# Kernel optimization log

Measured on AMD Instinct MI355X. Metric: run time of the kernel, lower is better.

## Reference

```python
import jax, jax.numpy as jnp
import numpy as np

NUM_HEADS = 8
HEAD_DIM = 64  # joiner_dim 512 / 8
LN_EPS = 1e-5


def _layer_norm(x, g, b):
    mu = jnp.mean(x, axis=-1, keepdims=True)
    var = jnp.mean(jnp.square(x - mu), axis=-1, keepdims=True)
    return (x - mu) * jax.lax.rsqrt(var + LN_EPS) * g + b


def setup_inputs() -> dict:
    key = jax.random.key(0)
    ks = jax.random.split(key, 24)
    N, T, S = 16, 512, 5
    E, D, J, V = 512, 512, 512, 2000
    s = 0.02
    inp = {
        "encoder_out": jax.random.normal(ks[0], (N, T, S, E), jnp.float32),
        "decoder_out": jax.random.normal(ks[1], (N, T, S, D), jnp.float32),
        # ScaledLinear projections (initial_scale absorbed into weights)
        "We": jax.random.normal(ks[2], (J, E), jnp.float32) * s * 0.25,
        "be": jnp.zeros((J,), jnp.float32),
        "Wd": jax.random.normal(ks[3], (J, D), jnp.float32) * s * 0.25,
        "bd": jnp.zeros((J,), jnp.float32),
        # LayerNorms
        "g_q": jnp.ones((J,), jnp.float32),
        "beta_q": jnp.zeros((J,), jnp.float32),
        "g_kv": jnp.ones((J,), jnp.float32),
        "beta_kv": jnp.zeros((J,), jnp.float32),
        # attention projections (xavier-ish)
        "Wq": jax.random.normal(ks[4], (J, J), jnp.float32) * s,
        "bq": jnp.zeros((J,), jnp.float32),
        "Wk": jax.random.normal(ks[5], (J, J), jnp.float32) * s,
        "bk": jnp.zeros((J,), jnp.float32),
        "Wv": jax.random.normal(ks[6], (J, J), jnp.float32) * s,
        "bv": jnp.zeros((J,), jnp.float32),
        "Wo": jax.random.normal(ks[7], (J, J), jnp.float32) * s,
        "bo": jnp.zeros((J,), jnp.float32),
        # final vocab projection
        "Wout": jax.random.normal(ks[8], (V, J), jnp.float32) * s,
        "bout": jnp.zeros((V,), jnp.float32),
    }
    return inp


def reference(encoder_out, decoder_out, We, be, Wd, bd, g_q, beta_q, g_kv, beta_kv,
              Wq, bq, Wk, bk, Wv, bv, Wo, bo, Wout, bout):
    # input projections (mode == "transducer", project_input=True)
    enc = jnp.einsum('ntsc,jc->ntsj', encoder_out, We) + be
    dec = jnp.einsum('ntsc,jc->ntsj', decoder_out, Wd) + bd

    # framewise sigmoid attention
    q_in = _layer_norm(dec, g_q, beta_q)
    kv_in = _layer_norm(enc, g_kv, beta_kv)
    q = jnp.einsum('ntsj,kj->ntsk', q_in, Wq) + bq
    k = jnp.einsum('ntsj,kj->ntsk', kv_in, Wk) + bk
    v = jnp.einsum('ntsj,kj->ntsk', kv_in, Wv) + bv

    shp = q.shape[:-1]
    q = q.reshape(*shp, NUM_HEADS, HEAD_DIM)
    k = k.reshape(*shp, NUM_HEADS, HEAD_DIM)
    v = v.reshape(*shp, NUM_HEADS, HEAD_DIM)

    scale = HEAD_DIM ** -0.5
    attn = jax.nn.sigmoid(jnp.sum(q * k, axis=-1, keepdims=True) * scale)  # (N,T,S,H,1)
    context = (attn * v).reshape(*shp, NUM_HEADS * HEAD_DIM)
    context = jnp.einsum('ntsj,kj->ntsk', context, Wo) + bo

    h = jnp.tanh(dec + context)
    logits = jnp.einsum('ntsj,vj->ntsv', h, Wout) + bout
    return logits
```

## Files before the change

kernel.cpp:

```cpp
#include <hip/hip_runtime.h>
#include <stdint.h>


typedef __attribute__((ext_vector_type(8))) __bf16 bf16x8;
typedef __attribute__((ext_vector_type(4))) float float4v;
typedef __attribute__((ext_vector_type(8))) unsigned short ushort8;

static constexpr int M_TOT = 16 * 512 * 5;
static constexpr int JDIM  = 512;
static constexpr int VOUT  = 2000;
static constexpr int VPAD  = 2048;

#define DI __device__ __forceinline__

DI float bf2f(unsigned short u) {
    union { unsigned int i; float f; } w; w.i = ((unsigned int)u) << 16; return w.f;
}
DI unsigned short f2bf(float f) {
    union { float f; unsigned int i; } w; w.f = f;
    return (unsigned short)((w.i + 0x8000u) >> 16);
}

DI void gld_lds16(const void* g, void* l) {
    __builtin_amdgcn_global_load_lds(
        reinterpret_cast<__attribute__((address_space(1))) void*>(
            reinterpret_cast<uintptr_t>(g)),
        reinterpret_cast<__attribute__((address_space(3))) void*>(
            reinterpret_cast<uintptr_t>(l)),
        16, 0, 0);
}

template <int EPI, int NOUT, bool A32>
__global__ __launch_bounds__(256) void gemm_bt(
    const void* __restrict__ Ap, const unsigned short* __restrict__ B,
    const float* __restrict__ bias, void* __restrict__ Cp,
    const unsigned short* __restrict__ dres,
    float* __restrict__ st_sum, float* __restrict__ st_ssq,
    const float* __restrict__ rs)
{
    constexpr int K = 512;
    constexpr int BM = 128, BN = 128, BK = 32;
    __shared__ unsigned short As[BM * BK];
    __shared__ unsigned short Bs[BN * BK];

    const int tid  = threadIdx.x;
    const int wave = tid >> 6;
    const int lane = tid & 63;
    const int wm   = wave >> 1;
    const int wn   = wave & 1;
    const int quad = lane >> 4;
    const int l16  = lane & 15;

    const int gx      = gridDim.x;
    const int nwg     = gx * gridDim.y;
    const int id      = blockIdx.x + gx * blockIdx.y;
    const int logical = (id & 7) * (nwg >> 3) + (id >> 3);
    const int m0 = (logical / gx) * BM;
    const int n0 = (logical % gx) * BN;

    float4v acc[4][4];
#pragma unroll
    for (int i = 0; i < 4; i++)
#pragma unroll
        for (int j = 0; j < 4; j++)
            acc[i][j] = {0.f, 0.f, 0.f, 0.f};

    const float*          Af = (const float*)Ap;
    const unsigned short* Ab = (const unsigned short*)Ap;

    const int c0 = tid, c1 = tid + 256;
    const int ar0 = c0 >> 2, ac0 = (c0 & 3) * 8;
    const int ar1 = c1 >> 2, ac1 = (c1 & 3) * 8;

    for (int k0 = 0; k0 < K; k0 += BK) {
        gld_lds16(&B[(size_t)(n0 + ar0) * K + k0 + ac0], &Bs[c0 * 8]);
        gld_lds16(&B[(size_t)(n0 + ar1) * K + k0 + ac1], &Bs[c1 * 8]);
        if constexpr (A32) {
            const float* p0 = &Af[(size_t)(m0 + ar0) * K + k0 + ac0];
            const float* p1 = &Af[(size_t)(m0 + ar1) * K + k0 + ac1];
            float4 f0 = *(const float4*)p0;
            float4 f1 = *(const float4*)(p0 + 4);
            float4 g0 = *(const float4*)p1;
            float4 g1 = *(const float4*)(p1 + 4);
            ushort8 u0, u1;
            u0[0] = f2bf(f0.x); u0[1] = f2bf(f0.y); u0[2] = f2bf(f0.z); u0[3] = f2bf(f0.w);
            u0[4] = f2bf(f1.x); u0[5] = f2bf(f1.y); u0[6] = f2bf(f1.z); u0[7] = f2bf(f1.w);
            u1[0] = f2bf(g0.x); u1[1] = f2bf(g0.y); u1[2] = f2bf(g0.z); u1[3] = f2bf(g0.w);
            u1[4] = f2bf(g1.x); u1[5] = f2bf(g1.y); u1[6] = f2bf(g1.z); u1[7] = f2bf(g1.w);
            *reinterpret_cast<ushort8*>(&As[c0 * 8]) = u0;
            *reinterpret_cast<ushort8*>(&As[c1 * 8]) = u1;
        } else {
            gld_lds16(&Ab[(size_t)(m0 + ar0) * K + k0 + ac0], &As[c0 * 8]);
            gld_lds16(&Ab[(size_t)(m0 + ar1) * K + k0 + ac1], &As[c1 * 8]);
        }
        __syncthreads();

        bf16x8 af[4], bfv[4];
#pragma unroll
        for (int i = 0; i < 4; i++)
            af[i] = *reinterpret_cast<const bf16x8*>(
                &As[(wm * 64 + i * 16 + l16) * BK + quad * 8]);
#pragma unroll
        for (int j = 0; j < 4; j++)
            bfv[j] = *reinterpret_cast<const bf16x8*>(
                &Bs[(wn * 64 + j * 16 + l16) * BK + quad * 8]);
#pragma unroll
        for (int i = 0; i < 4; i++)
#pragma unroll
            for (int j = 0; j < 4; j++)
                acc[i][j] = __builtin_amdgcn_mfma_f32_16x16x32_bf16(
                    af[i], bfv[j], acc[i][j], 0, 0, 0);
        __syncthreads();
    }

    float bias_v[4], rs_v[4];
#pragma unroll
    for (int j = 0; j < 4; j++) {
        int col = n0 + wn * 64 + j * 16 + l16;
        bias_v[j] = (col < NOUT) ? bias[col] : 0.f;
        if constexpr (EPI == 4) rs_v[j] = rs[col];
    }

    if constexpr (EPI == 4) {
#pragma unroll
        for (int i = 0; i < 4; i++) {
            int rbase = m0 + wm * 64 + i * 16 + quad * 4;
#pragma unroll
            for (int r = 0; r < 4; r++) {
                int row = rbase + r;
                float s  = st_sum[row];
                float s2 = st_ssq[row];
                float mean = s * (1.f / 512.f);
                float var  = s2 * (1.f / 512.f) - mean * mean;
                float rstd = rsqrtf(var + 1e-5f);
                float crow = -mean * rstd;
#pragma unroll
                for (int j = 0; j < 4; j++) {
                    int col = n0 + wn * 64 + j * 16 + l16;
                    float val = fmaf(rstd, acc[i][j][r],
                                fmaf(crow, rs_v[j], bias_v[j]));
                    ((unsigned short*)Cp)[(size_t)row * NOUT + col] = f2bf(val);
                }
            }
        }
    } else {
#pragma unroll
        for (int i = 0; i < 4; i++) {
            int rbase = m0 + wm * 64 + i * 16 + quad * 4;
#pragma unroll
            for (int j = 0; j < 4; j++) {
                int col = n0 + wn * 64 + j * 16 + l16;
#pragma unroll
                for (int r = 0; r < 4; r++) {
                    float val = acc[i][j][r] + bias_v[j];
                    int row = rbase + r;
                    if constexpr (EPI == 2) {
                        float d = bf2f(dres[(size_t)row * 512 + col]);
                        ((unsigned short*)Cp)[(size_t)row * 512 + col] = f2bf(tanhf(d + val));
                    } else if constexpr (EPI == 3) {
                        if (col < NOUT)
                            ((float*)Cp)[(size_t)row * NOUT + col] = val;
                    } else {
                        ((unsigned short*)Cp)[(size_t)row * NOUT + col] = f2bf(val);
                    }
                }
            }
        }
    }

    if constexpr (EPI == 6) {
#pragma unroll
        for (int i = 0; i < 4; i++) {
#pragma unroll
            for (int r = 0; r < 4; r++) {
                float ps = 0.f, ps2 = 0.f;
#pragma unroll
                for (int j = 0; j < 4; j++) {
                    float v = acc[i][j][r] + bias_v[j];
                    ps += v;
                    ps2 = fmaf(v, v, ps2);
                }
#pragma unroll
                for (int m = 1; m < 16; m <<= 1) {
                    ps  += __shfl_xor(ps,  m, 64);
                    ps2 += __shfl_xor(ps2, m, 64);
                }
                if (l16 == 0) {
                    int row = m0 + wm * 64 + i * 16 + quad * 4 + r;
                    atomicAdd(&st_sum[row], ps);
                    atomicAdd(&st_ssq[row], ps2);
                }
            }
        }
    }
}

__global__ __launch_bounds__(256) void wconv_kernel(
    const float* __restrict__ We, const float* __restrict__ Wd,
    const float* __restrict__ Wq, const float* __restrict__ Wk,
    const float* __restrict__ Wv, const float* __restrict__ Wo,
    const float* __restrict__ Wout,
    const float* __restrict__ g_q, const float* __restrict__ g_kv,
    unsigned short* __restrict__ WB, float* __restrict__ stz)
{
#pragma unroll
    for (int t = 0; t < 4; t++) {
        int i = blockIdx.x * 1024 + t * 256 + threadIdx.x;
        float v;
        if (i < 1572864) {
            int seg = i >> 18, off = i & 262143;
            const float* src = seg == 0 ? We : seg == 1 ? Wd : seg == 2 ? Wq
                             : seg == 3 ? Wk : seg == 4 ? Wv : Wo;
            v = src[off];
            int j = off & 511;
            if (seg == 2)                 v *= g_q[j];
            else if (seg == 3 || seg == 4) v *= g_kv[j];
        } else {
            int rem = i - 1572864;
            int row = rem >> 9;
            v = (row < VOUT) ? Wout[rem] : 0.f;
        }
        WB[i] = f2bf(v);
    }
    int z = blockIdx.x * 256 + threadIdx.x;
    if (z < 163840) stz[z] = 0.f;
}

__global__ __launch_bounds__(256) void lnprep_kernel(
    const float* __restrict__ Wq, const float* __restrict__ Wk,
    const float* __restrict__ Wv,
    const float* __restrict__ g_q, const float* __restrict__ beta_q,
    const float* __restrict__ g_kv, const float* __restrict__ beta_kv,
    const float* __restrict__ bq, const float* __restrict__ bk,
    const float* __restrict__ bv,
    float* __restrict__ rs_q, float* __restrict__ b_q,
    float* __restrict__ rs_kv, float* __restrict__ b_kv)
{
    int idx  = blockIdx.x * 4 + (threadIdx.x >> 6);
    int lane = threadIdx.x & 63;
    const float *W, *g, *bt, *bb; float *rs_out, *b_out; int r;
    if (idx < 512)       { W = Wq; g = g_q;  bt = beta_q;  bb = bq;
                           rs_out = &rs_q[idx];        b_out = &b_q[idx];        r = idx; }
    else if (idx < 1024) { W = Wk; g = g_kv; bt = beta_kv; bb = bk;
                           rs_out = &rs_kv[idx - 512]; b_out = &b_kv[idx - 512]; r = idx - 512; }
    else                 { W = Wv; g = g_kv; bt = beta_kv; bb = bv;
                           rs_out = &rs_kv[idx - 512]; b_out = &b_kv[idx - 512]; r = idx - 1024; }

    const float* wr = &W[(size_t)r * 512];
    float s = 0.f, sb = 0.f;
    int j0 = lane * 8;
    float4 w0 = *(const float4*)&wr[j0];
    float4 w1 = *(const float4*)&wr[j0 + 4];
    float4 ga = *(const float4*)&g[j0];
    float4 gb = *(const float4*)&g[j0 + 4];
    float4 ba = *(const float4*)&bt[j0];
    float4 bb4 = *(const float4*)&bt[j0 + 4];
    s  += w0.x * ga.x + w0.y * ga.y + w0.z * ga.z + w0.w * ga.w;
    s  += w1.x * gb.x + w1.y * gb.y + w1.z * gb.z + w1.w * gb.w;
    sb += w0.x * ba.x + w0.y * ba.y + w0.z * ba.z + w0.w * ba.w;
    sb += w1.x * bb4.x + w1.y * bb4.y + w1.z * bb4.z + w1.w * bb4.w;
#pragma unroll
    for (int m = 1; m < 64; m <<= 1) {
        s  += __shfl_xor(s,  m, 64);
        sb += __shfl_xor(sb, m, 64);
    }
    if (lane == 0) { *rs_out = s; *b_out = bb[r] + sb; }
}

__global__ __launch_bounds__(256) void attn_kernel(
    const unsigned short* __restrict__ q, const unsigned short* __restrict__ kv,
    unsigned short* __restrict__ ctx)
{
    int row  = blockIdx.x * 4 + (threadIdx.x >> 6);
    int lane = threadIdx.x & 63;
    size_t qoff = (size_t)row * 512 + lane * 8;
    size_t kvo  = (size_t)row * 1024 + lane * 8;
    ushort8 uq = *reinterpret_cast<const ushort8*>(&q[qoff]);
    ushort8 uk = *reinterpret_cast<const ushort8*>(&kv[kvo]);
    float dot = 0.f;
#pragma unroll
    for (int j = 0; j < 8; j++) dot += bf2f(uq[j]) * bf2f(uk[j]);
    dot += __shfl_xor(dot, 1, 64);
    dot += __shfl_xor(dot, 2, 64);
    dot += __shfl_xor(dot, 4, 64);
    float sg = 1.f / (1.f + __expf(-dot * 0.125f));
    ushort8 uv = *reinterpret_cast<const ushort8*>(&kv[kvo + 512]);
    ushort8 o;
#pragma unroll
    for (int j = 0; j < 8; j++) o[j] = f2bf(sg * bf2f(uv[j]));
    *reinterpret_cast<ushort8*>(&ctx[qoff]) = o;
}

extern "C" void kernel_launch(void* const* d_in, const int* in_sizes, int n_in,
                              void* d_out, int out_size, void* d_ws, size_t ws_size,
                              hipStream_t stream)
{
    (void)in_sizes; (void)n_in; (void)out_size; (void)ws_size;
    const float* enc_in  = (const float*)d_in[0];
    const float* dec_in  = (const float*)d_in[1];
    const float* We      = (const float*)d_in[2];  const float* be     = (const float*)d_in[3];
    const float* Wd      = (const float*)d_in[4];  const float* bd     = (const float*)d_in[5];
    const float* g_q     = (const float*)d_in[6];  const float* beta_q = (const float*)d_in[7];
    const float* g_kv    = (const float*)d_in[8];  const float* beta_kv= (const float*)d_in[9];
    const float* Wq      = (const float*)d_in[10]; const float* bq     = (const float*)d_in[11];
    const float* Wk      = (const float*)d_in[12]; const float* bk     = (const float*)d_in[13];
    const float* Wv      = (const float*)d_in[14]; const float* bv     = (const float*)d_in[15];
    const float* Wo      = (const float*)d_in[16]; const float* bo     = (const float*)d_in[17];
    const float* Wout    = (const float*)d_in[18]; const float* bout   = (const float*)d_in[19];
    float* out = (float*)d_out;

    unsigned short* WB    = (unsigned short*)d_ws;
    unsigned short* WeB   = WB + 0;
    unsigned short* WdB   = WB + 262144;
    unsigned short* WqB   = WB + 524288;
    unsigned short* WkB   = WB + 786432;
    unsigned short* WoB   = WB + 1310720;
    unsigned short* WoutB = WB + 1572864;

    char* sbase = (char*)d_ws + 5242880;
    const size_t SZ = (size_t)M_TOT * 512 * 2;
    unsigned short* S0 = (unsigned short*)(sbase + 0 * SZ);
    unsigned short* S1 = (unsigned short*)(sbase + 1 * SZ);
    unsigned short* S2 = (unsigned short*)(sbase + 2 * SZ);
    unsigned short* S3 = (unsigned short*)(sbase + 3 * SZ);
    unsigned short* S4 = (unsigned short*)(sbase + 4 * SZ);
    unsigned short* S5 = (unsigned short*)(sbase + 5 * SZ);

    float* stf  = (float*)(sbase + 5 * SZ);
    float* sumD = stf;
    float* ssqD = stf + 40960;
    float* sumE = stf + 81920;
    float* ssqE = stf + 122880;
    float* rs_q  = stf + 163840;
    float* b_q   = stf + 164352;
    float* rs_kv = stf + 164864;
    float* b_kv  = stf + 165888;

    dim3 blk(256);
    dim3 g512(JDIM / 128, M_TOT / 128);
    dim3 g1024(1024 / 128, M_TOT / 128);
    dim3 gout(VPAD / 128, M_TOT / 128);

    wconv_kernel<<<2560, blk, 0, stream>>>(We, Wd, Wq, Wk, Wv, Wo, Wout,
                                           g_q, g_kv, WB, stf);
    lnprep_kernel<<<384, blk, 0, stream>>>(Wq, Wk, Wv, g_q, beta_q, g_kv, beta_kv,
                                           bq, bk, bv, rs_q, b_q, rs_kv, b_kv);

    gemm_bt<6, 512, true><<<g512, blk, 0, stream>>>(enc_in, WeB, be, S0, nullptr,
                                                    sumE, ssqE, nullptr);
    gemm_bt<6, 512, true><<<g512, blk, 0, stream>>>(dec_in, WdB, bd, S1, nullptr,
                                                    sumD, ssqD, nullptr);

    gemm_bt<4, 512, false><<<g512, blk, 0, stream>>>(S1, WqB, b_q, S4, nullptr,
                                                     sumD, ssqD, rs_q);
    gemm_bt<4, 1024, false><<<g1024, blk, 0, stream>>>(S0, WkB, b_kv, S2, nullptr,
                                                       sumE, ssqE, rs_kv);

    attn_kernel<<<M_TOT / 4, blk, 0, stream>>>(S4, S2, S5);

    gemm_bt<2, 512, false><<<g512, blk, 0, stream>>>(S5, WoB, bo, S3, S1,
                                                     nullptr, nullptr, nullptr);

    gemm_bt<3, 2000, false><<<gout, blk, 0, stream>>>(S3, WoutB, bout, out, nullptr,
                                                      nullptr, nullptr, nullptr);
}
```

Before: 888.5 us.

## Pre-convert encoder/decoder inputs to bf16 in a merged prep kernel

Merges the weight-conversion and LN-prep kernels into one prep kernel that also converts the fp32 encoder and decoder inputs to bf16 buffers. The input-projection GEMMs can then stage A through direct global-to-LDS loads instead of fp32 register loads with inline conversion. The block swizzle becomes a template option and is kept only for the vocab GEMM. The cost is an extra full write and read of bf16 copies of both inputs, plus two more workspace buffers.

```diff
diff --git a/kernel.cpp b/kernel.cpp
--- a/kernel.cpp
+++ b/kernel.cpp
@@ -30,9 +30,9 @@
         16, 0, 0);
 }
 
-template <int EPI, int NOUT, bool A32>
+template <int EPI, int NOUT, bool SWZ>
 __global__ __launch_bounds__(256) void gemm_bt(
-    const void* __restrict__ Ap, const unsigned short* __restrict__ B,
+    const unsigned short* __restrict__ A, const unsigned short* __restrict__ B,
     const float* __restrict__ bias, void* __restrict__ Cp,
     const unsigned short* __restrict__ dres,
     float* __restrict__ st_sum, float* __restrict__ st_ssq,
@@ -51,10 +51,15 @@
     const int quad = lane >> 4;
     const int l16  = lane & 15;
 
-    const int gx      = gridDim.x;
-    const int nwg     = gx * gridDim.y;
-    const int id      = blockIdx.x + gx * blockIdx.y;
-    const int logical = (id & 7) * (nwg >> 3) + (id >> 3);
+    const int gx = gridDim.x;
+    const int id = blockIdx.x + gx * blockIdx.y;
+    int logical;
+    if constexpr (SWZ) {
+        const int nwg = gx * gridDim.y;
+        logical = (id & 7) * (nwg >> 3) + (id >> 3);
+    } else {
+        logical = id;
+    }
     const int m0 = (logical / gx) * BM;
     const int n0 = (logical % gx) * BN;
 
@@ -64,9 +69,6 @@
 #pragma unroll
         for (int j = 0; j < 4; j++)
             acc[i][j] = {0.f, 0.f, 0.f, 0.f};
-
-    const float*          Af = (const float*)Ap;
-    const unsigned short* Ab = (const unsigned short*)Ap;
 
     const int c0 = tid, c1 = tid + 256;
     const int ar0 = c0 >> 2, ac0 = (c0 & 3) * 8;
@@ -75,24 +77,8 @@
     for (int k0 = 0; k0 < K; k0 += BK) {
         gld_lds16(&B[(size_t)(n0 + ar0) * K + k0 + ac0], &Bs[c0 * 8]);
         gld_lds16(&B[(size_t)(n0 + ar1) * K + k0 + ac1], &Bs[c1 * 8]);
-        if constexpr (A32) {
-            const float* p0 = &Af[(size_t)(m0 + ar0) * K + k0 + ac0];
-            const float* p1 = &Af[(size_t)(m0 + ar1) * K + k0 + ac1];
-            float4 f0 = *(const float4*)p0;
-            float4 f1 = *(const float4*)(p0 + 4);
-            float4 g0 = *(const float4*)p1;
-            float4 g1 = *(const float4*)(p1 + 4);
-            ushort8 u0, u1;
-            u0[0] = f2bf(f0.x); u0[1] = f2bf(f0.y); u0[2] = f2bf(f0.z); u0[3] = f2bf(f0.w);
-            u0[4] = f2bf(f1.x); u0[5] = f2bf(f1.y); u0[6] = f2bf(f1.z); u0[7] = f2bf(f1.w);
-            u1[0] = f2bf(g0.x); u1[1] = f2bf(g0.y); u1[2] = f2bf(g0.z); u1[3] = f2bf(g0.w);
-            u1[4] = f2bf(g1.x); u1[5] = f2bf(g1.y); u1[6] = f2bf(g1.z); u1[7] = f2bf(g1.w);
-            *reinterpret_cast<ushort8*>(&As[c0 * 8]) = u0;
-            *reinterpret_cast<ushort8*>(&As[c1 * 8]) = u1;
-        } else {
-            gld_lds16(&Ab[(size_t)(m0 + ar0) * K + k0 + ac0], &As[c0 * 8]);
-            gld_lds16(&Ab[(size_t)(m0 + ar1) * K + k0 + ac1], &As[c1 * 8]);
-        }
+        gld_lds16(&A[(size_t)(m0 + ar0) * K + k0 + ac0], &As[c0 * 8]);
+        gld_lds16(&A[(size_t)(m0 + ar1) * K + k0 + ac1], &As[c1 * 8]);
         __syncthreads();
 
         bf16x8 af[4], bfv[4];
@@ -195,76 +181,105 @@
     }
 }
 
-__global__ __launch_bounds__(256) void wconv_kernel(
+__global__ __launch_bounds__(256) void prep_kernel(
     const float* __restrict__ We, const float* __restrict__ Wd,
     const float* __restrict__ Wq, const float* __restrict__ Wk,
     const float* __restrict__ Wv, const float* __restrict__ Wo,
     const float* __restrict__ Wout,
-    const float* __restrict__ g_q, const float* __restrict__ g_kv,
-    unsigned short* __restrict__ WB, float* __restrict__ stz)
-{
-#pragma unroll
-    for (int t = 0; t < 4; t++) {
-        int i = blockIdx.x * 1024 + t * 256 + threadIdx.x;
-        float v;
-        if (i < 1572864) {
-            int seg = i >> 18, off = i & 262143;
-            const float* src = seg == 0 ? We : seg == 1 ? Wd : seg == 2 ? Wq
-                             : seg == 3 ? Wk : seg == 4 ? Wv : Wo;
-            v = src[off];
-            int j = off & 511;
-            if (seg == 2)                 v *= g_q[j];
-            else if (seg == 3 || seg == 4) v *= g_kv[j];
-        } else {
-            int rem = i - 1572864;
-            int row = rem >> 9;
-            v = (row < VOUT) ? Wout[rem] : 0.f;
-        }
-        WB[i] = f2bf(v);
-    }
-    int z = blockIdx.x * 256 + threadIdx.x;
-    if (z < 163840) stz[z] = 0.f;
-}
-
-__global__ __launch_bounds__(256) void lnprep_kernel(
-    const float* __restrict__ Wq, const float* __restrict__ Wk,
-    const float* __restrict__ Wv,
     const float* __restrict__ g_q, const float* __restrict__ beta_q,
     const float* __restrict__ g_kv, const float* __restrict__ beta_kv,
     const float* __restrict__ bq, const float* __restrict__ bk,
     const float* __restrict__ bv,
+    const float* __restrict__ enc_in, const float* __restrict__ dec_in,
+    unsigned short* __restrict__ WB,
+    unsigned short* __restrict__ encB, unsigned short* __restrict__ decB,
+    float* __restrict__ stz,
     float* __restrict__ rs_q, float* __restrict__ b_q,
     float* __restrict__ rs_kv, float* __restrict__ b_kv)
 {
-    int idx  = blockIdx.x * 4 + (threadIdx.x >> 6);
-    int lane = threadIdx.x & 63;
-    const float *W, *g, *bt, *bb; float *rs_out, *b_out; int r;
-    if (idx < 512)       { W = Wq; g = g_q;  bt = beta_q;  bb = bq;
-                           rs_out = &rs_q[idx];        b_out = &b_q[idx];        r = idx; }
-    else if (idx < 1024) { W = Wk; g = g_kv; bt = beta_kv; bb = bk;
-                           rs_out = &rs_kv[idx - 512]; b_out = &b_kv[idx - 512]; r = idx - 512; }
-    else                 { W = Wv; g = g_kv; bt = beta_kv; bb = bv;
-                           rs_out = &rs_kv[idx - 512]; b_out = &b_kv[idx - 512]; r = idx - 1024; }
-
-    const float* wr = &W[(size_t)r * 512];
-    float s = 0.f, sb = 0.f;
-    int j0 = lane * 8;
-    float4 w0 = *(const float4*)&wr[j0];
-    float4 w1 = *(const float4*)&wr[j0 + 4];
-    float4 ga = *(const float4*)&g[j0];
-    float4 gb = *(const float4*)&g[j0 + 4];
-    float4 ba = *(const float4*)&bt[j0];
-    float4 bb4 = *(const float4*)&bt[j0 + 4];
-    s  += w0.x * ga.x + w0.y * ga.y + w0.z * ga.z + w0.w * ga.w;
-    s  += w1.x * gb.x + w1.y * gb.y + w1.z * gb.z + w1.w * gb.w;
-    sb += w0.x * ba.x + w0.y * ba.y + w0.z * ba.z + w0.w * ba.w;
-    sb += w1.x * bb4.x + w1.y * bb4.y + w1.z * bb4.z + w1.w * bb4.w;
-#pragma unroll
-    for (int m = 1; m < 64; m <<= 1) {
-        s  += __shfl_xor(s,  m, 64);
-        sb += __shfl_xor(sb, m, 64);
-    }
-    if (lane == 0) { *rs_out = s; *b_out = bb[r] + sb; }
+    const int b   = blockIdx.x;
+    const int tid = threadIdx.x;
+
+    if (b < 1280) {
+        if (b < 768) {
+            const int seg = b >> 7;
+            const int off = (b & 127) * 2048 + tid * 8;
+            const float* src = seg == 0 ? We : seg == 1 ? Wd : seg == 2 ? Wq
+                             : seg == 3 ? Wk : seg == 4 ? Wv : Wo;
+            float4 f0 = *(const float4*)&src[off];
+            float4 f1 = *(const float4*)&src[off + 4];
+            float sc[8] = {1,1,1,1,1,1,1,1};
+            if (seg >= 2 && seg <= 4) {
+                const float* g = (seg == 2) ? g_q : g_kv;
+                int j0 = off & 511;
+                float4 s0 = *(const float4*)&g[j0];
+                float4 s1 = *(const float4*)&g[j0 + 4];
+                sc[0]=s0.x; sc[1]=s0.y; sc[2]=s0.z; sc[3]=s0.w;
+                sc[4]=s1.x; sc[5]=s1.y; sc[6]=s1.z; sc[7]=s1.w;
+            }
+            ushort8 u;
+            u[0]=f2bf(f0.x*sc[0]); u[1]=f2bf(f0.y*sc[1]); u[2]=f2bf(f0.z*sc[2]); u[3]=f2bf(f0.w*sc[3]);
+            u[4]=f2bf(f1.x*sc[4]); u[5]=f2bf(f1.y*sc[5]); u[6]=f2bf(f1.z*sc[6]); u[7]=f2bf(f1.w*sc[7]);
+            *reinterpret_cast<ushort8*>(&WB[(size_t)b * 2048 + tid * 8]) = u;
+        } else {
+            const int rem = (b - 768) * 2048 + tid * 8;
+            const int row = rem >> 9;
+            ushort8 u;
+            if (row < VOUT) {
+                float4 f0 = *(const float4*)&Wout[rem];
+                float4 f1 = *(const float4*)&Wout[rem + 4];
+                u[0]=f2bf(f0.x); u[1]=f2bf(f0.y); u[2]=f2bf(f0.z); u[3]=f2bf(f0.w);
+                u[4]=f2bf(f1.x); u[5]=f2bf(f1.y); u[6]=f2bf(f1.z); u[7]=f2bf(f1.w);
+            } else {
+                u = (ushort8)0;
+            }
+            *reinterpret_cast<ushort8*>(&WB[1572864 + (size_t)(b - 768) * 2048 + tid * 8]) = u;
+        }
+        int z = b * 256 + tid;
+        if (z < 163840) stz[z] = 0.f;
+    } else if (b < 21760) {
+        const bool isDec = b >= 11520;
+        const int  cb    = b - (isDec ? 11520 : 1280);
+        const float* src = isDec ? dec_in : enc_in;
+        unsigned short* dst = isDec ? decB : encB;
+        const size_t base = (size_t)cb * 2048 + tid * 8;
+        float4 f0 = *(const float4*)&src[base];
+        float4 f1 = *(const float4*)&src[base + 4];
+        ushort8 u;
+        u[0]=f2bf(f0.x); u[1]=f2bf(f0.y); u[2]=f2bf(f0.z); u[3]=f2bf(f0.w);
+        u[4]=f2bf(f1.x); u[5]=f2bf(f1.y); u[6]=f2bf(f1.z); u[7]=f2bf(f1.w);
+        *reinterpret_cast<ushort8*>(&dst[base]) = u;
+    } else {
+        const int idx  = (b - 21760) * 4 + (tid >> 6);
+        const int lane = tid & 63;
+        const float *W, *g, *bt, *bb; float *rs_out, *b_out; int r;
+        if (idx < 512)       { W = Wq; g = g_q;  bt = beta_q;  bb = bq;
+                               rs_out = &rs_q[idx];        b_out = &b_q[idx];        r = idx; }
+        else if (idx < 1024) { W = Wk; g = g_kv; bt = beta_kv; bb = bk;
+                               rs_out = &rs_kv[idx - 512]; b_out = &b_kv[idx - 512]; r = idx - 512; }
+        else                 { W = Wv; g = g_kv; bt = beta_kv; bb = bv;
+                               rs_out = &rs_kv[idx - 512]; b_out = &b_kv[idx - 512]; r = idx - 1024; }
+
+        const float* wr = &W[(size_t)r * 512];
+        float s = 0.f, sb = 0.f;
+        int j0 = lane * 8;
+        float4 w0 = *(const float4*)&wr[j0];
+        float4 w1 = *(const float4*)&wr[j0 + 4];
+        float4 ga = *(const float4*)&g[j0];
+        float4 gb = *(const float4*)&g[j0 + 4];
+        float4 ba = *(const float4*)&bt[j0];
+        float4 bb4 = *(const float4*)&bt[j0 + 4];
+        s  += w0.x * ga.x + w0.y * ga.y + w0.z * ga.z + w0.w * ga.w;
+        s  += w1.x * gb.x + w1.y * gb.y + w1.z * gb.z + w1.w * gb.w;
+        sb += w0.x * ba.x + w0.y * ba.y + w0.z * ba.z + w0.w * ba.w;
+        sb += w1.x * bb4.x + w1.y * bb4.y + w1.z * bb4.z + w1.w * bb4.w;
+#pragma unroll
+        for (int m = 1; m < 64; m <<= 1) {
+            s  += __shfl_xor(s,  m, 64);
+            sb += __shfl_xor(sb, m, 64);
+        }
+        if (lane == 0) { *rs_out = s; *b_out = bb[r] + sb; }
+    }
 }
 
 __global__ __launch_bounds__(256) void attn_kernel(
@@ -319,18 +334,20 @@
 
     char* sbase = (char*)d_ws + 5242880;
     const size_t SZ = (size_t)M_TOT * 512 * 2;
-    unsigned short* S0 = (unsigned short*)(sbase + 0 * SZ);
-    unsigned short* S1 = (unsigned short*)(sbase + 1 * SZ);
-    unsigned short* S2 = (unsigned short*)(sbase + 2 * SZ);
-    unsigned short* S3 = (unsigned short*)(sbase + 3 * SZ);
-    unsigned short* S4 = (unsigned short*)(sbase + 4 * SZ);
-    unsigned short* S5 = (unsigned short*)(sbase + 5 * SZ);
-
-    float* stf  = (float*)(sbase + 5 * SZ);
-    float* sumD = stf;
-    float* ssqD = stf + 40960;
-    float* sumE = stf + 81920;
-    float* ssqE = stf + 122880;
+    unsigned short* EB = (unsigned short*)(sbase + 0 * SZ);
+    unsigned short* DB = (unsigned short*)(sbase + 1 * SZ);
+    unsigned short* S0 = (unsigned short*)(sbase + 2 * SZ);
+    unsigned short* S1 = (unsigned short*)(sbase + 3 * SZ);
+    unsigned short* S2 = (unsigned short*)(sbase + 4 * SZ);
+    unsigned short* S3 = (unsigned short*)(sbase + 5 * SZ);
+    unsigned short* S4 = (unsigned short*)(sbase + 6 * SZ);
+    unsigned short* S5 = (unsigned short*)(sbase + 7 * SZ);
+
+    float* stf  = (float*)(sbase + 7 * SZ);
+    float* sumE = stf;
+    float* ssqE = stf + 40960;
+    float* sumD = stf + 81920;
+    float* ssqD = stf + 122880;
     float* rs_q  = stf + 163840;
     float* b_q   = stf + 164352;
     float* rs_kv = stf + 164864;
@@ -341,15 +358,14 @@
     dim3 g1024(1024 / 128, M_TOT / 128);
     dim3 gout(VPAD / 128, M_TOT / 128);
 
-    wconv_kernel<<<2560, blk, 0, stream>>>(We, Wd, Wq, Wk, Wv, Wo, Wout,
-                                           g_q, g_kv, WB, stf);
-    lnprep_kernel<<<384, blk, 0, stream>>>(Wq, Wk, Wv, g_q, beta_q, g_kv, beta_kv,
-                                           bq, bk, bv, rs_q, b_q, rs_kv, b_kv);
-
-    gemm_bt<6, 512, true><<<g512, blk, 0, stream>>>(enc_in, WeB, be, S0, nullptr,
-                                                    sumE, ssqE, nullptr);
-    gemm_bt<6, 512, true><<<g512, blk, 0, stream>>>(dec_in, WdB, bd, S1, nullptr,
-                                                    sumD, ssqD, nullptr);
+    prep_kernel<<<22144, blk, 0, stream>>>(
+        We, Wd, Wq, Wk, Wv, Wo, Wout, g_q, beta_q, g_kv, beta_kv,
+        bq, bk, bv, enc_in, dec_in, WB, EB, DB, stf, rs_q, b_q, rs_kv, b_kv);
+
+    gemm_bt<6, 512, false><<<g512, blk, 0, stream>>>(EB, WeB, be, S0, nullptr,
+                                                     sumE, ssqE, nullptr);
+    gemm_bt<6, 512, false><<<g512, blk, 0, stream>>>(DB, WdB, bd, S1, nullptr,
+                                                     sumD, ssqD, nullptr);
 
     gemm_bt<4, 512, false><<<g512, blk, 0, stream>>>(S1, WqB, b_q, S4, nullptr,
                                                      sumD, ssqD, rs_q);
@@ -361,6 +377,6 @@
     gemm_bt<2, 512, false><<<g512, blk, 0, stream>>>(S5, WoB, bo, S3, S1,
                                                      nullptr, nullptr, nullptr);
 
-    gemm_bt<3, 2000, false><<<gout, blk, 0, stream>>>(S3, WoutB, bout, out, nullptr,
-                                                      nullptr, nullptr, nullptr);
-}
+    gemm_bt<3, 2000, true><<<gout, blk, 0, stream>>>(S3, WoutB, bout, out, nullptr,
+                                                     nullptr, nullptr, nullptr);
+}
```

Result: slower. 916.6 us (+3.2%).
